# Kernel tuning notes

Hardware: AMD Instinct MI355X
Metric: run time of the kernel (lower is better)

The kernel has to match this reference:

```python
import jax, jax.numpy as jnp
import numpy as np

BIN_SIZE = 256  # init arg bin_size
K = 16          # init arg k


def setup_inputs() -> dict:
    key = jax.random.key(0)
    k1, k2 = jax.random.split(key)
    x = jax.random.normal(k1, (2, 8192, 256), dtype=jnp.float32)          # (B, N, D)
    codebook = jax.random.normal(k2, (256, 32), dtype=jnp.float32)        # (D, max_num_bins//2)
    return {"x": x, "codebook": codebook}


def reference(x, codebook):
    B, N, D = x.shape
    n_bins = N // BIN_SIZE
    # LSH binning: project onto random hyperplanes, argmax over [proj, -proj]
    mul = jnp.matmul(x, codebook[:, : n_bins // 2])          # (B, N, n_bins//2)
    cmul = jnp.concatenate([mul, -mul], axis=-1)             # (B, N, n_bins)
    bin_idx = jnp.argmax(cmul, axis=-1)                      # (B, N)
    # stable sort points by bin id -> equal-size bins (matches torch.argsort)
    bins_split = jnp.argsort(bin_idx, axis=-1).reshape(B, n_bins, BIN_SIZE)
    # gather points into bins
    pts = jnp.take_along_axis(x, bins_split.reshape(B, N, 1), axis=1)
    pts = pts.reshape(B, n_bins, BIN_SIZE, D)
    # per-bin dense similarity + sigmoid
    dm = jax.nn.sigmoid(jnp.einsum('bnid,bnjd->bnik'.replace('k', 'j'), pts, pts))  # (B, n_bins, BIN, BIN)
    vals, inds = jax.lax.top_k(dm, K)                        # (B, n_bins, BIN, K)
    # map local bin indices back to global point indices
    flat_split = bins_split.reshape(B, N)
    bin_off = jnp.arange(n_bins, dtype=inds.dtype)[None, :, None, None] * BIN_SIZE
    gdst = jnp.take_along_axis(flat_split, (bin_off + inds).reshape(B, -1), axis=1)
    gdst = gdst.reshape(B, n_bins, BIN_SIZE, K)
    gsrc = jnp.broadcast_to(bins_split[..., None], vals.shape)
    bidx = jnp.broadcast_to(jnp.arange(B)[:, None, None, None], vals.shape)
    # coalesced sparse adjacency, represented densely (duplicates summed like coalesce())
    out = jnp.zeros((B, N, N), x.dtype).at[bidx, gsrc, gdst].add(vals)
    return out
```

## Files before the change

kernel.cpp:

```cpp
#include <hip/hip_runtime.h>
#include <math.h>

#define BB    2
#define NN    8192
#define DD    256
#define NBINS 32
#define BINSZ 256
#define NPROJ 16
#define TOPK  16
#define NPTS  (BB * NN)

typedef float vf4 __attribute__((ext_vector_type(4)));

__global__ __launch_bounds__(256) void k_bins_fill(const float* __restrict__ x,
                                                   const float* __restrict__ cb,
                                                   int* __restrict__ bin_idx,
                                                   float* __restrict__ out) {
    __shared__ double cbd[DD][NPROJ];
    const int t   = threadIdx.x;
    const int bid = blockIdx.x;

    for (int q = t; q < DD * 4; q += 256) {
        int d = q >> 2, j4 = q & 3;
        float4 v = *(const float4*)(cb + d * 32 + j4 * 4);
        cbd[d][j4 * 4 + 0] = (double)v.x;
        cbd[d][j4 * 4 + 1] = (double)v.y;
        cbd[d][j4 * 4 + 2] = (double)v.z;
        cbd[d][j4 * 4 + 3] = (double)v.w;
    }
    __syncthreads();

    if (t < 64) {
        const int p = bid * 64 + t;
        const float* xr = x + (size_t)p * DD;

        double a[NPROJ];
#pragma unroll
        for (int j = 0; j < NPROJ; ++j) a[j] = 0.0;

        for (int d0 = 0; d0 < DD; d0 += 4) {
            float4 xv = *(const float4*)(xr + d0);
            float xs[4] = {xv.x, xv.y, xv.z, xv.w};
#pragma unroll
            for (int dd = 0; dd < 4; ++dd) {
                double xd = (double)xs[dd];
#pragma unroll
                for (int j = 0; j < NPROJ; ++j)
                    a[j] = fma(cbd[d0 + dd][j], xd, a[j]);
            }
        }

        float bv = -INFINITY; int bj = 0;
#pragma unroll
        for (int j = 0; j < NPROJ; ++j) {
            float m = (float)a[j];
            if (m > bv) { bv = m; bj = j; }
        }
#pragma unroll
        for (int j = 0; j < NPROJ; ++j) {
            float m = -(float)a[j];
            if (m > bv) { bv = m; bj = j + NPROJ; }
        }
        bin_idx[p] = bj;
    }

    {
        const float4 z4 = make_float4(0.f, 0.f, 0.f, 0.f);
        float4* ob = (float4*)out + (size_t)bid * 131072;
#pragma unroll 4
        for (int j = t; j < 131072; j += 256)
            ob[j] = z4;
    }
}

__global__ __launch_bounds__(256) void k_sort(const int* __restrict__ bin_idx,
                                              int* __restrict__ order) {
    __shared__ int c[NBINS][256];
    __shared__ int base[NBINS];
    const int t = threadIdx.x;
    const int b = blockIdx.x;
    const int* bi = bin_idx + b * NN;

    for (int j = 0; j < NBINS; ++j) c[j][t] = 0;
    __syncthreads();

    const int i0 = t * 32;
    for (int i = 0; i < 32; ++i) c[bi[i0 + i]][t]++;
    __syncthreads();

    if (t < NBINS) {
        int s = 0;
        for (int q = 0; q < 256; ++q) s += c[t][q];
        base[t] = s;
    }
    __syncthreads();
    if (t == 0) {
        int run = 0;
        for (int j = 0; j < NBINS; ++j) { int tmp = base[j]; base[j] = run; run += tmp; }
    }
    __syncthreads();
    if (t < NBINS) {
        int run = base[t];
        for (int q = 0; q < 256; ++q) { int tmp = c[t][q]; c[t][q] = run; run += tmp; }
    }
    __syncthreads();

    int* ob = order + b * NN;
    for (int i = 0; i < 32; ++i) {
        int gi = i0 + i;
        int bb = bi[gi];
        int pos = c[bb][t]++;
        ob[pos] = gi;
    }
}

#define RT 32
__global__ __launch_bounds__(256, 2) void k_sim(const float* __restrict__ x,
                                                const int* __restrict__ order,
                                                float* __restrict__ out) {
    __shared__ int   idx[BINSZ];
    __shared__ float As[RT][260];
    __shared__ float S[RT][BINSZ + 1];
    __shared__ float tvs[RT][TOPK];
    __shared__ int   tds[RT][TOPK];

    const int t   = threadIdx.x;
    const int bid = blockIdx.x;
    const int b   = bid >> 8;
    const int bin = (bid >> 3) & 31;
    const int r0  = (bid & 7) * RT;

    idx[t] = order[b * NN + bin * BINSZ + t];
    __syncthreads();

    const float* xb = x + (size_t)b * NN * DD;

    {
        const int ar = t >> 3;
        const int ac = t & 7;
        const float* ag = xb + (size_t)idx[r0 + ar] * DD;
#pragma unroll
        for (int q = 0; q < 8; ++q) {
            float4 v = *(const float4*)(ag + (ac + 8 * q) * 4);
            *(float4*)&As[ar][(ac + 8 * q) * 4] = v;
        }
    }

    const int rg    = t >> 6;
    const int cbase = t & 63;
    const float* colp[4];
#pragma unroll
    for (int k = 0; k < 4; ++k)
        colp[k] = xb + (size_t)idx[cbase + 64 * k] * DD;

    double acc[8][4];
#pragma unroll
    for (int r = 0; r < 8; ++r)
#pragma unroll
        for (int k = 0; k < 4; ++k) acc[r][k] = 0.0;

    __syncthreads();

#pragma unroll 1
    for (int it = 0; it < 16; ++it) {
        const int k0 = it * 16;
        float4 bv[4][4];
#pragma unroll
        for (int k = 0; k < 4; ++k)
#pragma unroll
            for (int q = 0; q < 4; ++q)
                bv[k][q] = *(const float4*)(colp[k] + k0 + q * 4);

#pragma unroll
        for (int dd4 = 0; dd4 < 4; ++dd4) {
            float4 af[8];
#pragma unroll
            for (int rr = 0; rr < 8; ++rr)
                af[rr] = *(const float4*)&As[rg * 8 + rr][k0 + dd4 * 4];
            const float4 b0 = bv[0][dd4], b1 = bv[1][dd4],
                         b2 = bv[2][dd4], b3 = bv[3][dd4];
#pragma unroll
            for (int e = 0; e < 4; ++e) {
                const double be0 = (double)((e == 0) ? b0.x : (e == 1) ? b0.y : (e == 2) ? b0.z : b0.w);
                const double be1 = (double)((e == 0) ? b1.x : (e == 1) ? b1.y : (e == 2) ? b1.z : b1.w);
                const double be2 = (double)((e == 0) ? b2.x : (e == 1) ? b2.y : (e == 2) ? b2.z : b2.w);
                const double be3 = (double)((e == 0) ? b3.x : (e == 1) ? b3.y : (e == 2) ? b3.z : b3.w);
#pragma unroll
                for (int rr = 0; rr < 8; ++rr) {
                    const float ae = (e == 0) ? af[rr].x : (e == 1) ? af[rr].y
                                   : (e == 2) ? af[rr].z : af[rr].w;
                    const double ad = (double)ae;
                    acc[rr][0] = fma(ad, be0, acc[rr][0]);
                    acc[rr][1] = fma(ad, be1, acc[rr][1]);
                    acc[rr][2] = fma(ad, be2, acc[rr][2]);
                    acc[rr][3] = fma(ad, be3, acc[rr][3]);
                }
            }
        }
    }

#pragma unroll
    for (int rr = 0; rr < 8; ++rr)
#pragma unroll
        for (int k = 0; k < 4; ++k) {
            float s32 = (float)acc[rr][k];
            S[rg * 8 + rr][cbase + 64 * k] = 1.0f / (1.0f + expf(-s32));
        }
    __syncthreads();

    if (t < RT) {
        float tv[TOPK]; int ti[TOPK];
#pragma unroll
        for (int q = 0; q < TOPK; ++q) { tv[q] = -INFINITY; ti[q] = 0; }
        for (int cc = 0; cc < BINSZ; ++cc) {
            float v = S[t][cc];
            if (v > tv[TOPK - 1]) {
                tv[TOPK - 1] = v; ti[TOPK - 1] = cc;
#pragma unroll
                for (int q = TOPK - 1; q > 0; --q) {
                    if (tv[q] > tv[q - 1]) {
                        float fv = tv[q]; tv[q] = tv[q - 1]; tv[q - 1] = fv;
                        int   fi = ti[q]; ti[q] = ti[q - 1]; ti[q - 1] = fi;
                    }
                }
            }
        }
#pragma unroll
        for (int q = 0; q < TOPK; ++q) {
            tvs[t][q] = tv[q];
            tds[t][q] = idx[ti[q]];
        }
    }
    __syncthreads();

    for (int p = t; p < RT * TOPK; p += 256) {
        int r = p >> 4, q = p & 15;
        float* orow = out + ((size_t)b * NN + idx[r0 + r]) * NN;
        orow[tds[r][q]] = tvs[r][q];
    }
}

extern "C" void kernel_launch(void* const* d_in, const int* in_sizes, int n_in,
                              void* d_out, int out_size, void* d_ws, size_t ws_size,
                              hipStream_t stream) {
    const float* x  = (const float*)d_in[0];
    const float* cb = (const float*)d_in[1];
    float* out      = (float*)d_out;

    int* bin_idx = (int*)d_ws;
    int* order   = bin_idx + NPTS;

    k_bins_fill<<<256, 256, 0, stream>>>(x, cb, bin_idx, out);
    k_sort<<<BB, 256, 0, stream>>>(bin_idx, order);
    k_sim<<<BB * NBINS * 8, 256, 0, stream>>>(x, order, out);
}
```

Baseline: 698.8 us.

## Split output zero-fill across bin, sort and similarity kernels to overlap compute

The 512 MB output zeroing is no longer done entirely in the first kernel. Rows 0-1279 are zeroed in k_bins_fill, rows 1280-2559 by 256 extra blocks added to the sort launch, and every remaining row is zeroed inside k_sim with nontemporal stores, interleaved with its FP64 GEMM loop. The aim is to hide the bandwidth-bound fill behind compute, since k_sort used only 2 blocks and k_sim is compute-bound. Each row is zeroed by the k_sim block that later writes its top-k entries, so ordering within the block matters. The split of rows depends on hardcoded thresholds.

```diff
diff --git a/kernel.cpp b/kernel.cpp
--- a/kernel.cpp
+++ b/kernel.cpp
@@ -10,6 +10,9 @@
 #define TOPK  16
 #define NPTS  (BB * NN)
 
+#define F1 1280
+#define F2 2560
+
 typedef float vf4 __attribute__((ext_vector_type(4)));
 
 __global__ __launch_bounds__(256) void k_bins_fill(const float* __restrict__ x,
@@ -30,6 +33,17 @@
     }
     __syncthreads();
 
+    {
+        const vf4 z4 = (vf4)0.0f;
+#pragma unroll
+        for (int q = 0; q < 5; ++q) {
+            vf4* orow = (vf4*)(out + (size_t)(bid * 5 + q) * NN);
+#pragma unroll
+            for (int j = 0; j < 8; ++j)
+                orow[j * 256 + t] = z4;
+        }
+    }
+
     if (t < 64) {
         const int p = bid * 64 + t;
         const float* xr = x + (size_t)p * DD;
@@ -63,22 +77,29 @@
         }
         bin_idx[p] = bj;
     }
-
-    {
-        const float4 z4 = make_float4(0.f, 0.f, 0.f, 0.f);
-        float4* ob = (float4*)out + (size_t)bid * 131072;
-#pragma unroll 4
-        for (int j = t; j < 131072; j += 256)
-            ob[j] = z4;
-    }
-}
-
-__global__ __launch_bounds__(256) void k_sort(const int* __restrict__ bin_idx,
-                                              int* __restrict__ order) {
+}
+
+__global__ __launch_bounds__(256) void k_sort_fill(const int* __restrict__ bin_idx,
+                                                   int* __restrict__ order,
+                                                   float* __restrict__ out) {
+    const int t   = threadIdx.x;
+    const int bid = blockIdx.x;
+
+    if (bid >= 2) {
+        const vf4 z4 = (vf4)0.0f;
+#pragma unroll
+        for (int q = 0; q < 5; ++q) {
+            vf4* orow = (vf4*)(out + (size_t)(F1 + (bid - 2) * 5 + q) * NN);
+#pragma unroll
+            for (int j = 0; j < 8; ++j)
+                orow[j * 256 + t] = z4;
+        }
+        return;
+    }
+
     __shared__ int c[NBINS][256];
     __shared__ int base[NBINS];
-    const int t = threadIdx.x;
-    const int b = blockIdx.x;
+    const int b = bid;
     const int* bi = bin_idx + b * NN;
 
     for (int j = 0; j < NBINS; ++j) c[j][t] = 0;
@@ -159,17 +180,34 @@
 #pragma unroll
         for (int k = 0; k < 4; ++k) acc[r][k] = 0.0;
 
+    const vf4 z4 = (vf4)0.0f;
+
     __syncthreads();
 
 #pragma unroll 1
     for (int it = 0; it < 16; ++it) {
         const int k0 = it * 16;
+
         float4 bv[4][4];
 #pragma unroll
         for (int k = 0; k < 4; ++k)
 #pragma unroll
             for (int q = 0; q < 4; ++q)
                 bv[k][q] = *(const float4*)(colp[k] + k0 + q * 4);
+
+        {
+            const int zr = it * 2;
+#pragma unroll
+            for (int rr = 0; rr < 2; ++rr) {
+                const int pid = idx[r0 + zr + rr];
+                if (b * NN + pid >= F2) {
+                    vf4* orow = (vf4*)(out + ((size_t)b * NN + pid) * NN);
+#pragma unroll
+                    for (int j = 0; j < 8; ++j)
+                        __builtin_nontemporal_store(z4, orow + j * 256 + t);
+                }
+            }
+        }
 
 #pragma unroll
         for (int dd4 = 0; dd4 < 4; ++dd4) {
@@ -251,6 +289,6 @@
     int* order   = bin_idx + NPTS;
 
     k_bins_fill<<<256, 256, 0, stream>>>(x, cb, bin_idx, out);
-    k_sort<<<BB, 256, 0, stream>>>(bin_idx, order);
+    k_sort_fill<<<258, 256, 0, stream>>>(bin_idx, order, out);
     k_sim<<<BB * NBINS * 8, 256, 0, stream>>>(x, order, out);
 }
```

New measurement: 652.0 us. 1.07x faster.
